# Kernel tuning notes

Measured on AMD Instinct MI355X. Metric: run time of the kernel, lower is better.

Reference implementation:

```python
import jax, jax.numpy as jnp
import numpy as np

N_NODES = 50000
N_EDGES = 800000
D = 128
H = 128


def setup_inputs() -> dict:
    key = jax.random.key(0)
    ks = jax.random.split(key, 8)
    s = 1.0 / np.sqrt(D)
    return {
        "x": jax.random.normal(ks[0], (N_NODES, D), dtype=jnp.float32),
        "edge_index": jax.random.randint(ks[1], (2, N_EDGES), 0, N_NODES, dtype=jnp.int64),
        "W1_l": jax.random.normal(ks[2], (D, H), dtype=jnp.float32) * s,
        "b1_l": jax.random.normal(ks[3], (H,), dtype=jnp.float32) * s,
        "W1_r": jax.random.normal(ks[4], (D, H), dtype=jnp.float32) * s,
        "W2_l": jax.random.normal(ks[5], (H, H), dtype=jnp.float32) * s,
        "b2_l": jax.random.normal(ks[6], (H,), dtype=jnp.float32) * s,
        "W2_r": jax.random.normal(ks[7], (H, H), dtype=jnp.float32) * s,
    }


def _sage_conv(x, src, dst, W_l, b_l, W_r, n_nodes):
    # mean aggregation of source features at destination nodes
    agg = jax.ops.segment_sum(x[src], dst, num_segments=n_nodes)          # [N, d]
    cnt = jax.ops.segment_sum(jnp.ones((src.shape[0],), x.dtype), dst,
                              num_segments=n_nodes)                        # [N]
    mean = agg / jnp.maximum(cnt, 1.0)[:, None]
    out = mean @ W_l + b_l + x @ W_r                                       # [N, h]
    # L2 normalize (normalize=True in SAGEConv)
    norm = jnp.linalg.norm(out, axis=-1, keepdims=True)
    return out / jnp.maximum(norm, 1e-12)


def reference(x, edge_index, W1_l, b1_l, W1_r, W2_l, b2_l, W2_r):
    src, dst = edge_index[0], edge_index[1]
    n = x.shape[0]
    h = jax.nn.relu(_sage_conv(x, src, dst, W1_l, b1_l, W1_r, n))
    h = jax.nn.relu(_sage_conv(h, src, dst, W2_l, b2_l, W2_r, n))
    return h
```

## Files before the change

### kernel.cpp

```cpp
#include <hip/hip_runtime.h>

#define N_NODES 50000
#define N_EDGES 800000
#define CAP 48

typedef __bf16 bf16_t;
typedef bf16_t bf16x8 __attribute__((ext_vector_type(8)));
typedef float f32x16 __attribute__((ext_vector_type(16)));

union Frag { float4 f4; bf16x8 h; };
union Pack8 { ushort u[8]; float4 f4; };

__device__ __forceinline__ ushort f2bf(float f) {
    unsigned u = __float_as_uint(f);
    return (ushort)((u + 0x7fffu + ((u >> 16) & 1u)) >> 16);
}
__device__ __forceinline__ float bf2f(unsigned bits) {
    return __uint_as_float(bits << 16);
}

__global__ void detect_kernel(const int* __restrict__ idx, int* __restrict__ flag) {
    int t = threadIdx.x;
    int v = idx[2 * t + 1];
    unsigned long long b = __ballot(v == 0);
    if (t == 0) *flag = (b == 0xFFFFFFFFFFFFFFFFull) ? 1 : 0;
}

__device__ __forceinline__ void load_edge(const int* __restrict__ idx, int f, int e,
                                          int& src, int& dst) {
    if (f) { src = idx[2 * e]; dst = idx[2 * N_EDGES + 2 * e]; }
    else   { src = idx[e];     dst = idx[N_EDGES + e]; }
}

__global__ __launch_bounds__(256) void prep_kernel(
        const float2* __restrict__ X, uint* __restrict__ Xb,
        int* __restrict__ deg,
        const float* __restrict__ W1l, const float* __restrict__ W1r,
        const float* __restrict__ W2l, const float* __restrict__ W2r,
        ushort* __restrict__ Bp) {
    int i = blockIdx.x * 256 + threadIdx.x;
    if (i < N_NODES * 64) {
        float2 v = X[i];
        Xb[i] = ((uint)f2bf(v.y) << 16) | (uint)f2bf(v.x);
    }
    if (i < N_NODES) deg[i] = 0;
    if (i < 8192) {
        int layer = i >> 12;
        int rec   = i & 4095;
        int t = rec >> 10;
        int s = (rec >> 6) & 15;
        int l = rec & 63;
        const float* Wl = layer ? W2l : W1l;
        const float* Wr = layer ? W2r : W1r;
        int n = t * 32 + (l & 31);
        int kb = s * 16 + (l >> 5) * 8;
        Pack8 o;
#pragma unroll
        for (int j = 0; j < 8; ++j) {
            int k = kb + j;
            float v = (k < 128) ? Wl[k * 128 + n] : Wr[(k - 128) * 128 + n];
            o.u[j] = f2bf(v);
        }
        *(float4*)(Bp + (size_t)i * 8) = o.f4;
    }
}

__global__ void bin_fixed_kernel(const int* __restrict__ idx,
                                 const int* __restrict__ flag,
                                 int* __restrict__ deg,
                                 ushort* __restrict__ esrc) {
    int e = blockIdx.x * blockDim.x + threadIdx.x;
    if (e >= N_EDGES) return;
    int f = *flag, src, dst;
    load_edge(idx, f, e, src, dst);
    int pos = atomicAdd(&deg[dst], 1);
    if (pos < CAP) esrc[dst * CAP + pos] = (ushort)src;
}

__global__ __launch_bounds__(256) void gather_mean_kernel(
        const uint2* __restrict__ X2, const int* __restrict__ deg,
        const ushort* __restrict__ esrc, uint2* __restrict__ mean2) {
    const int wave = threadIdx.x >> 6;
    const int lane = threadIdx.x & 63;
    const int node = blockIdx.x * 8 + wave * 2 + (lane >> 5);
    const int l = lane & 31;
    if (node >= N_NODES) return;
    int dg = deg[node];
    if (dg > CAP) dg = CAP;
    const ushort* es = esrc + node * CAP;

    float c0[4] = {0, 0, 0, 0}, c1[4] = {0, 0, 0, 0};
    float c2[4] = {0, 0, 0, 0}, c3[4] = {0, 0, 0, 0};
    int p = 0;
    for (; p + 3 < dg; p += 4) {
        ushort4 ss = *(const ushort4*)(es + p);
        uint2 v0 = X2[(size_t)ss.x * 32 + l];
        uint2 v1 = X2[(size_t)ss.y * 32 + l];
        uint2 v2 = X2[(size_t)ss.z * 32 + l];
        uint2 v3 = X2[(size_t)ss.w * 32 + l];
        c0[0] += bf2f(v0.x & 0xffff); c0[1] += bf2f(v0.x >> 16);
        c0[2] += bf2f(v0.y & 0xffff); c0[3] += bf2f(v0.y >> 16);
        c1[0] += bf2f(v1.x & 0xffff); c1[1] += bf2f(v1.x >> 16);
        c1[2] += bf2f(v1.y & 0xffff); c1[3] += bf2f(v1.y >> 16);
        c2[0] += bf2f(v2.x & 0xffff); c2[1] += bf2f(v2.x >> 16);
        c2[2] += bf2f(v2.y & 0xffff); c2[3] += bf2f(v2.y >> 16);
        c3[0] += bf2f(v3.x & 0xffff); c3[1] += bf2f(v3.x >> 16);
        c3[2] += bf2f(v3.y & 0xffff); c3[3] += bf2f(v3.y >> 16);
    }
    for (; p < dg; ++p) {
        uint2 v = X2[(size_t)es[p] * 32 + l];
        c0[0] += bf2f(v.x & 0xffff); c0[1] += bf2f(v.x >> 16);
        c0[2] += bf2f(v.y & 0xffff); c0[3] += bf2f(v.y >> 16);
    }
    const float inv = 1.0f / (float)max(dg, 1);
    const float m0 = (c0[0] + c1[0] + c2[0] + c3[0]) * inv;
    const float m1 = (c0[1] + c1[1] + c2[1] + c3[1]) * inv;
    const float m2 = (c0[2] + c1[2] + c2[2] + c3[2]) * inv;
    const float m3 = (c0[3] + c1[3] + c2[3] + c3[3]) * inv;
    uint2 m;
    m.x = ((uint)f2bf(m1) << 16) | (uint)f2bf(m0);
    m.y = ((uint)f2bf(m3) << 16) | (uint)f2bf(m2);
    mean2[(size_t)node * 32 + l] = m;
}

template<bool OUT_F32>
__global__ __launch_bounds__(256) void gemm_mfma_kernel(
        const ushort* __restrict__ Amean, const ushort* Aself,
        const ushort* __restrict__ Bpack, const float* __restrict__ bias,
        void* Yout) {
    __shared__ float rs[2][64];
    const int tid = threadIdx.x;
    const int w = tid >> 6, l = tid & 63;
    const int lr = l & 31, lh = l >> 5;
    const int mrow0 = blockIdx.x * 64 + (w & 1) * 32;
    const int t0 = (w >> 1) * 2;

    f32x16 acc0, acc1;
#pragma unroll
    for (int i = 0; i < 16; ++i) { acc0[i] = 0.0f; acc1[i] = 0.0f; }

#pragma unroll
    for (int s = 0; s < 16; ++s) {
        const ushort* Ab = (s < 8) ? Amean : Aself;
        Frag a, b0, b1;
        a.f4  = *(const float4*)(Ab + (size_t)(mrow0 + lr) * 128 + (s & 7) * 16 + lh * 8);
        b0.f4 = *(const float4*)(Bpack + (size_t)(((t0) * 16 + s) * 64 + l) * 8);
        b1.f4 = *(const float4*)(Bpack + (size_t)(((t0 + 1) * 16 + s) * 64 + l) * 8);
        acc0 = __builtin_amdgcn_mfma_f32_32x32x16_bf16(a.h, b0.h, acc0, 0, 0, 0);
        acc1 = __builtin_amdgcn_mfma_f32_32x32x16_bf16(a.h, b1.h, acc1, 0, 0, 0);
    }

    const float bia0 = bias[t0 * 32 + lr];
    const float bia1 = bias[t0 * 32 + 32 + lr];
    float sq[16];
#pragma unroll
    for (int r = 0; r < 16; ++r) {
        float v0 = acc0[r] + bia0;
        float v1 = acc1[r] + bia1;
        acc0[r] = v0; acc1[r] = v1;
        float s_ = v0 * v0 + v1 * v1;
        s_ += __shfl_xor(s_, 1);
        s_ += __shfl_xor(s_, 2);
        s_ += __shfl_xor(s_, 4);
        s_ += __shfl_xor(s_, 8);
        s_ += __shfl_xor(s_, 16);
        sq[r] = s_;
    }
    if (lr == 0) {
#pragma unroll
        for (int r = 0; r < 16; ++r) {
            int rowl = (w & 1) * 32 + (r & 3) + 8 * (r >> 2) + 4 * lh;
            rs[w >> 1][rowl] = sq[r];
        }
    }
    __syncthreads();
#pragma unroll
    for (int r = 0; r < 16; ++r) {
        int rowl = (w & 1) * 32 + (r & 3) + 8 * (r >> 2) + 4 * lh;
        int grow = blockIdx.x * 64 + rowl;
        float tot = rs[0][rowl] + rs[1][rowl];
        float sc = 1.0f / fmaxf(sqrtf(tot), 1e-12f);
        if (grow < N_NODES) {
            float o0 = fmaxf(acc0[r] * sc, 0.0f);
            float o1 = fmaxf(acc1[r] * sc, 0.0f);
            if (OUT_F32) {
                float* Y = (float*)Yout;
                Y[(size_t)grow * 128 + t0 * 32 + lr]      = o0;
                Y[(size_t)grow * 128 + t0 * 32 + 32 + lr] = o1;
            } else {
                ushort* Y = (ushort*)Yout;
                Y[(size_t)grow * 128 + t0 * 32 + lr]      = f2bf(o0);
                Y[(size_t)grow * 128 + t0 * 32 + 32 + lr] = f2bf(o1);
            }
        }
    }
}

extern "C" void kernel_launch(void* const* d_in, const int* in_sizes, int n_in,
                              void* d_out, int out_size, void* d_ws, size_t ws_size,
                              hipStream_t stream) {
    const float* x    = (const float*)d_in[0];
    const int*   idx  = (const int*)d_in[1];
    const float* W1l  = (const float*)d_in[2];
    const float* b1l  = (const float*)d_in[3];
    const float* W1r  = (const float*)d_in[4];
    const float* W2l  = (const float*)d_in[5];
    const float* b2l  = (const float*)d_in[6];
    const float* W2r  = (const float*)d_in[7];
    float* out = (float*)d_out;

    int*    deg   = (int*)d_ws;
    int*    flag  = deg + N_NODES;
    ushort* esrc  = (ushort*)((int*)d_ws + 50016);
    uint*   meanb = (uint*)((int*)d_ws + 1250016);
    uint*   xh    = (uint*)((int*)d_ws + 4450016);
    ushort* Bp    = (ushort*)((int*)d_ws + 7650016);

    detect_kernel<<<1, 64, 0, stream>>>(idx, flag);
    prep_kernel<<<(N_NODES * 64 + 255) / 256, 256, 0, stream>>>(
        (const float2*)x, xh, deg, W1l, W1r, W2l, W2r, Bp);
    bin_fixed_kernel<<<(N_EDGES + 255) / 256, 256, 0, stream>>>(idx, flag, deg, esrc);

    const int gb = (N_NODES + 7) / 8;
    const int mb = (N_NODES + 63) / 64;

    gather_mean_kernel<<<gb, 256, 0, stream>>>(
        (const uint2*)xh, deg, esrc, (uint2*)meanb);
    gemm_mfma_kernel<false><<<mb, 256, 0, stream>>>(
        (const ushort*)meanb, (const ushort*)xh, Bp, b1l, (void*)xh);
    gather_mean_kernel<<<gb, 256, 0, stream>>>(
        (const uint2*)xh, deg, esrc, (uint2*)meanb);
    gemm_mfma_kernel<true><<<mb, 256, 0, stream>>>(
        (const ushort*)meanb, (const ushort*)xh, Bp + 4096 * 8, b2l, (void*)out);
}
```

Baseline: 235.6 us.

## Replace global-atomic edge binning with histogram, scan, scatter and LDS list build

Edge-list construction no longer does 800k global atomics into a fixed-capacity per-node array. It now runs a tiled counting sort: a per-tile histogram over 256 node bins (fused into the prep kernel), a scan, a stable scatter into bin segments, and a per-bin build in shared memory that writes deg and coalesced esrc rows. Detection of the index dtype is folded in, which drops one launch. This aims to remove scattered global atomics and uncoalesced 2-byte writes, at the cost of more kernel launches and an extra pass over the edge indices.

After: 220.2 us. -6.6%, faster.

```diff
diff --git a/kernel.cpp b/kernel.cpp
--- a/kernel.cpp
+++ b/kernel.cpp
@@ -4,6 +4,12 @@
 #define N_EDGES 800000
 #define CAP 48
 
+#define TILE   2048
+#define NT     391
+#define NT_PAD 392
+#define NB     256
+#define BIN_NODES 196
+
 typedef __bf16 bf16_t;
 typedef bf16_t bf16x8 __attribute__((ext_vector_type(8)));
 typedef float f32x16 __attribute__((ext_vector_type(16)));
@@ -19,11 +25,11 @@
     return __uint_as_float(bits << 16);
 }
 
-__global__ void detect_kernel(const int* __restrict__ idx, int* __restrict__ flag) {
-    int t = threadIdx.x;
-    int v = idx[2 * t + 1];
+__device__ __forceinline__ int detect_i64(const int* __restrict__ idx) {
+    int lane = threadIdx.x & 63;
+    int v = idx[2 * lane + 1];
     unsigned long long b = __ballot(v == 0);
-    if (t == 0) *flag = (b == 0xFFFFFFFFFFFFFFFFull) ? 1 : 0;
+    return (b == 0xFFFFFFFFFFFFFFFFull) ? 1 : 0;
 }
 
 __device__ __forceinline__ void load_edge(const int* __restrict__ idx, int f, int e,
@@ -31,50 +37,150 @@
     if (f) { src = idx[2 * e]; dst = idx[2 * N_EDGES + 2 * e]; }
     else   { src = idx[e];     dst = idx[N_EDGES + e]; }
 }
-
-__global__ __launch_bounds__(256) void prep_kernel(
+__device__ __forceinline__ int load_dst(const int* __restrict__ idx, int f, int e) {
+    return f ? idx[2 * N_EDGES + 2 * e] : idx[N_EDGES + e];
+}
+
+#define XBLK ((N_NODES * 64 + 255) / 256)
+__global__ __launch_bounds__(256) void prep_hist_kernel(
         const float2* __restrict__ X, uint* __restrict__ Xb,
-        int* __restrict__ deg,
         const float* __restrict__ W1l, const float* __restrict__ W1r,
         const float* __restrict__ W2l, const float* __restrict__ W2r,
-        ushort* __restrict__ Bp) {
-    int i = blockIdx.x * 256 + threadIdx.x;
-    if (i < N_NODES * 64) {
-        float2 v = X[i];
-        Xb[i] = ((uint)f2bf(v.y) << 16) | (uint)f2bf(v.x);
-    }
-    if (i < N_NODES) deg[i] = 0;
-    if (i < 8192) {
-        int layer = i >> 12;
-        int rec   = i & 4095;
-        int t = rec >> 10;
-        int s = (rec >> 6) & 15;
-        int l = rec & 63;
-        const float* Wl = layer ? W2l : W1l;
-        const float* Wr = layer ? W2r : W1r;
-        int n = t * 32 + (l & 31);
-        int kb = s * 16 + (l >> 5) * 8;
-        Pack8 o;
-#pragma unroll
-        for (int j = 0; j < 8; ++j) {
-            int k = kb + j;
-            float v = (k < 128) ? Wl[k * 128 + n] : Wr[(k - 128) * 128 + n];
-            o.u[j] = f2bf(v);
-        }
-        *(float4*)(Bp + (size_t)i * 8) = o.f4;
-    }
-}
-
-__global__ void bin_fixed_kernel(const int* __restrict__ idx,
-                                 const int* __restrict__ flag,
-                                 int* __restrict__ deg,
-                                 ushort* __restrict__ esrc) {
-    int e = blockIdx.x * blockDim.x + threadIdx.x;
-    if (e >= N_EDGES) return;
-    int f = *flag, src, dst;
-    load_edge(idx, f, e, src, dst);
-    int pos = atomicAdd(&deg[dst], 1);
-    if (pos < CAP) esrc[dst * CAP + pos] = (ushort)src;
+        ushort* __restrict__ Bp,
+        const int* __restrict__ idx, uint* __restrict__ hist) {
+    if (blockIdx.x < XBLK) {
+        int i = blockIdx.x * 256 + threadIdx.x;
+        if (i < N_NODES * 64) {
+            float2 v = X[i];
+            Xb[i] = ((uint)f2bf(v.y) << 16) | (uint)f2bf(v.x);
+        }
+        if (i < 8192) {
+            int layer = i >> 12;
+            int rec   = i & 4095;
+            int t = rec >> 10;
+            int s = (rec >> 6) & 15;
+            int l = rec & 63;
+            const float* Wl = layer ? W2l : W1l;
+            const float* Wr = layer ? W2r : W1r;
+            int n = t * 32 + (l & 31);
+            int kb = s * 16 + (l >> 5) * 8;
+            Pack8 o;
+#pragma unroll
+            for (int j = 0; j < 8; ++j) {
+                int k = kb + j;
+                float v = (k < 128) ? Wl[k * 128 + n] : Wr[(k - 128) * 128 + n];
+                o.u[j] = f2bf(v);
+            }
+            *(float4*)(Bp + (size_t)i * 8) = o.f4;
+        }
+        return;
+    }
+    __shared__ uint h[NB];
+    const int t   = blockIdx.x - XBLK;
+    const int tid = threadIdx.x;
+    h[tid] = 0;
+    int f = detect_i64(idx);
+    __syncthreads();
+    const int e0 = t * TILE;
+    const int e1 = min(e0 + TILE, N_EDGES);
+    for (int e = e0 + tid; e < e1; e += 256) {
+        int dst = load_dst(idx, f, e);
+        atomicAdd(&h[(uint)dst / BIN_NODES], 1u);
+    }
+    __syncthreads();
+    hist[(size_t)tid * NT_PAD + t] = h[tid];
+}
+
+__global__ __launch_bounds__(64) void scan_kernel(
+        const uint* __restrict__ hist, uint* __restrict__ base,
+        uint* __restrict__ total) {
+    const int b = blockIdx.x;
+    const int lane = threadIdx.x;
+    uint run = 0;
+    for (int c = 0; c < NT; c += 64) {
+        int t = c + lane;
+        uint v = (t < NT) ? hist[(size_t)b * NT_PAD + t] : 0u;
+        uint x = v;
+#pragma unroll
+        for (int d = 1; d < 64; d <<= 1) {
+            uint y = __shfl_up(x, d);
+            if (lane >= d) x += y;
+        }
+        if (t < NT) base[(size_t)b * NT_PAD + t] = run + (x - v);
+        run += __shfl(x, 63);
+    }
+    if (lane == 0) total[b] = run;
+}
+
+__global__ __launch_bounds__(256) void scatter_kernel(
+        const int* __restrict__ idx, const uint* __restrict__ base,
+        const uint* __restrict__ total, uint* __restrict__ eseg) {
+    __shared__ uint s[NB];
+    __shared__ uint binoff[NB];
+    __shared__ uint lh[NB];
+    const int t = blockIdx.x, tid = threadIdx.x;
+    int f = detect_i64(idx);
+    uint tot = total[tid];
+    s[tid] = tot;
+    __syncthreads();
+#pragma unroll
+    for (int d = 1; d < NB; d <<= 1) {
+        uint v = (tid >= d) ? s[tid - d] : 0u;
+        __syncthreads();
+        s[tid] += v;
+        __syncthreads();
+    }
+    binoff[tid] = (s[tid] - tot) + base[(size_t)tid * NT_PAD + t];
+    lh[tid] = 0;
+    __syncthreads();
+    const int e0 = t * TILE;
+    const int e1 = min(e0 + TILE, N_EDGES);
+    for (int e = e0 + tid; e < e1; e += 256) {
+        int src, dst;
+        load_edge(idx, f, e, src, dst);
+        uint b  = (uint)dst / BIN_NODES;
+        uint dl = (uint)dst - b * BIN_NODES;
+        uint r  = atomicAdd(&lh[b], 1u);
+        eseg[binoff[b] + r] = (uint)src | (dl << 16);
+    }
+}
+
+__global__ __launch_bounds__(256) void build_kernel(
+        const uint* __restrict__ eseg, const uint* __restrict__ total,
+        int* __restrict__ deg, ushort* __restrict__ esrc) {
+    __shared__ uint s[NB];
+    __shared__ uint cnt[BIN_NODES];
+    __shared__ __align__(16) ushort lists[BIN_NODES * CAP];
+    const int b = blockIdx.x, tid = threadIdx.x;
+    uint tot = total[tid];
+    s[tid] = tot;
+    __syncthreads();
+#pragma unroll
+    for (int d = 1; d < NB; d <<= 1) {
+        uint v = (tid >= d) ? s[tid - d] : 0u;
+        __syncthreads();
+        s[tid] += v;
+        __syncthreads();
+    }
+    const uint start = (b == 0) ? 0u : s[b - 1];
+    const uint cntb  = s[b] - start;
+    for (int i = tid; i < BIN_NODES; i += 256) cnt[i] = 0;
+    __syncthreads();
+    for (uint i = tid; i < cntb; i += 256) {
+        uint p  = eseg[start + i];
+        uint dl = p >> 16;
+        uint r  = atomicAdd(&cnt[dl], 1u);
+        if (r < CAP) lists[dl * CAP + r] = (ushort)(p & 0xffffu);
+    }
+    __syncthreads();
+    const int node0 = b * BIN_NODES;
+    const int valid = min(BIN_NODES, N_NODES - node0);
+    for (int i = tid; i < valid; i += 256)
+        deg[node0 + i] = (int)cnt[i];
+    const int nvec = valid * 6;
+    uint4* dst4 = (uint4*)(esrc + (size_t)node0 * CAP);
+    const uint4* src4 = (const uint4*)lists;
+    for (int i = tid; i < nvec; i += 256) dst4[i] = src4[i];
 }
 
 __global__ __launch_bounds__(256) void gather_mean_kernel(
@@ -210,16 +316,20 @@
     float* out = (float*)d_out;
 
     int*    deg   = (int*)d_ws;
-    int*    flag  = deg + N_NODES;
     ushort* esrc  = (ushort*)((int*)d_ws + 50016);
+    uint*   hist  = (uint*)((int*)d_ws + 50016);
+    uint*   base  = hist + NB * NT_PAD;
     uint*   meanb = (uint*)((int*)d_ws + 1250016);
+    uint*   eseg  = meanb;
+    uint*   total = meanb + 800000;
     uint*   xh    = (uint*)((int*)d_ws + 4450016);
     ushort* Bp    = (ushort*)((int*)d_ws + 7650016);
 
-    detect_kernel<<<1, 64, 0, stream>>>(idx, flag);
-    prep_kernel<<<(N_NODES * 64 + 255) / 256, 256, 0, stream>>>(
-        (const float2*)x, xh, deg, W1l, W1r, W2l, W2r, Bp);
-    bin_fixed_kernel<<<(N_EDGES + 255) / 256, 256, 0, stream>>>(idx, flag, deg, esrc);
+    prep_hist_kernel<<<XBLK + NT, 256, 0, stream>>>(
+        (const float2*)x, xh, W1l, W1r, W2l, W2r, Bp, idx, hist);
+    scan_kernel<<<NB, 64, 0, stream>>>(hist, base, total);
+    scatter_kernel<<<NT, 256, 0, stream>>>(idx, base, total, eseg);
+    build_kernel<<<NB, 256, 0, stream>>>(eseg, total, deg, esrc);
 
     const int gb = (N_NODES + 7) / 8;
     const int mb = (N_NODES + 63) / 64;
```
